# Performance work log

Measured on AMD Instinct MI355X. Metric: run time of the kernel, lower is better.

## Reference

```python
import jax, jax.numpy as jnp
import numpy as np

EPS = 1e-6
OMEGA = 0.1


def setup_inputs() -> dict:
    key = jax.random.key(0)
    k1, k2 = jax.random.split(key)
    n, d, kk = 4096, 128, 4
    inputs = jax.random.uniform(k1, (n, d), dtype=jnp.float32)  # positive so log(sim) is finite
    labels = jax.random.randint(k2, (n, kk), 0, 64, dtype=jnp.int64)
    return {"inputs": inputs, "labels": labels}


def reference(inputs, labels):
    n, kk = labels.shape
    sim = inputs @ inputs.T                      # [n, n]
    logsim = jnp.log(sim + EPS)                  # a_{jk} = log(sim[j,k]+eps)
    targets = labels[:, 0]
    eye = jnp.eye(n, dtype=bool)
    # pos_mask[j,k] = (targets[j] == targets[k]) xor diagonal
    pos = (targets[:, None] == targets[None, :]) & ~eye
    # eq[j,l,i] = (labels[l,i] == targets[j])
    eq = targets[:, None, None] == labels[None, :, :]
    m_idx = jnp.arange(kk)
    cols = kk - 1 - m_idx                        # neg_mask[m] uses label column kk-1-m
    # neg_mask[m][j,l] == 1  <=>  ~eq[j,l,kk-1-m]  AND  (m==0 or eq[j,l,kk-m])
    neq_col = ~eq[:, :, cols]                    # [j,l,m]
    prev_ok = jnp.concatenate(
        [jnp.ones((n, n, 1), dtype=bool), eq[:, :, cols[:-1]]], axis=-1)
    neg = neq_col & prev_ok                      # [j,l,m]
    # loss_pair[m] = log(Omega+eps) - log(Omega^(kk-m+1)+eps)
    lp = jnp.log(OMEGA + EPS) - jnp.log(OMEGA ** (kk - m_idx + 1) + EPS)  # [kk]
    dt = logsim.dtype
    posf = pos.astype(dt)
    negf = neg.astype(dt)
    # term = (a_jk - b_jlm)^2 with b_jlm = logsim[j,l] + 0.1*lp[m]
    # expand: sum_jklm pos*neg*(a^2 - 2ab + b^2), separable over k and (l,m)
    c = posf.sum(1)                              # [j] count of positives
    S1 = (posf * logsim).sum(1)                  # [j] sum a
    S2 = (posf * logsim ** 2).sum(1)             # [j] sum a^2
    b = logsim[:, :, None] + 0.1 * lp[None, None, :]   # [j,l,m]
    Ncnt = negf.sum(1)                           # [j,m]
    T1 = (negf * b).sum(1)                       # [j,m]
    T2 = (negf * b ** 2).sum(1)                  # [j,m]
    loss = (S2[:, None] * Ncnt - 2.0 * S1[:, None] * T1 + c[:, None] * T2).sum()
    return loss
```

## Files before the change

### kernel.cpp

```cpp
#include <hip/hip_runtime.h>
#include <math.h>

constexpr int N   = 4096;
constexpr int D   = 128;
constexpr int LDK = D + 8;
constexpr int NT  = 64;

typedef __attribute__((ext_vector_type(8))) short short8;
typedef __attribute__((ext_vector_type(4))) float floatx4;

__device__ inline unsigned short f2bf(float f) {
  unsigned u = __builtin_bit_cast(unsigned, f);
  u = (u + 0x7FFFu + ((u >> 16) & 1u)) >> 16;
  return (unsigned short)u;
}

__global__ __launch_bounds__(256) void build_coef(
    const int* __restrict__ labels, float4* __restrict__ tab,
    float B0, float B1, float B2, float B3,
    float Q0, float Q1, float Q2, float Q3) {
  const int idx = blockIdx.x * 256 + threadIdx.x;
  const int t = idx >> 12;
  const int j = idx & (N - 1);
  const int4 L = ((const int4*)labels)[j];
  const bool e0 = (t == L.x), e1 = (t == L.y), e2 = (t == L.z), e3 = (t == L.w);
  const bool n0 = !e3, n1 = e3 && !e2, n2 = e2 && !e1, n3 = e1 && !e0;
  const float g0 = (float)((n0 ? 1 : 0) + (n1 ? 1 : 0) + (n2 ? 1 : 0) + (n3 ? 1 : 0));
  const float gB = (n0 ? B0 : 0.f) + (n1 ? B1 : 0.f) + (n2 ? B2 : 0.f) + (n3 ? B3 : 0.f);
  const float gQ = (n0 ? Q0 : 0.f) + (n1 ? Q1 : 0.f) + (n2 ? Q2 : 0.f) + (n3 ? Q3 : 0.f);
  tab[idx] = make_float4(gB, gQ, g0, e0 ? 1.f : 0.f);
}

__global__ __launch_bounds__(256, 2) void logratio_phaseA(
    const float* __restrict__ inputs, const int* __restrict__ labels,
    const float4* __restrict__ tab, float* __restrict__ part) {

  __shared__ __align__(16) char smem[2 * 128 * LDK * 2];
  unsigned short* As = (unsigned short*)smem;
  unsigned short* Bs = As + 128 * LDK;
  float* Red = (float*)smem;

  const int tid = threadIdx.x;
  const int iBase = blockIdx.y * 128;
  const int jBase = blockIdx.x * 128;

#pragma unroll
  for (int p = 0; p < 16; ++p) {
    const int idx = p * 256 + tid;
    const int row = idx >> 5;
    const int cf  = idx & 31;
    const float4 va = *(const float4*)&inputs[(iBase + row) * D + cf * 4];
    uint2 wa;
    wa.x = (unsigned)f2bf(va.x) | ((unsigned)f2bf(va.y) << 16);
    wa.y = (unsigned)f2bf(va.z) | ((unsigned)f2bf(va.w) << 16);
    *(uint2*)&As[row * LDK + cf * 4] = wa;
    const float4 vb = *(const float4*)&inputs[(jBase + row) * D + cf * 4];
    uint2 wb;
    wb.x = (unsigned)f2bf(vb.x) | ((unsigned)f2bf(vb.y) << 16);
    wb.y = (unsigned)f2bf(vb.z) | ((unsigned)f2bf(vb.w) << 16);
    *(uint2*)&Bs[row * LDK + cf * 4] = wb;
  }
  __syncthreads();

  const int w    = tid >> 6;
  const int lane = tid & 63;
  const int lc   = lane & 15;
  const int quad = lane >> 4;

  floatx4 acc[2][8] = {};
  const unsigned short* Abase = As + (w * 32 + lc) * LDK + quad * 8;
  const unsigned short* Bbase = Bs + lc * LDK + quad * 8;

#pragma unroll
  for (int kb = 0; kb < 4; ++kb) {
    short8 af[2], bfr[8];
    af[0] = *(const short8*)(Abase + kb * 32);
    af[1] = *(const short8*)(Abase + 16 * LDK + kb * 32);
#pragma unroll
    for (int tn = 0; tn < 8; ++tn)
      bfr[tn] = *(const short8*)(Bbase + tn * 16 * LDK + kb * 32);
#pragma unroll
    for (int tm = 0; tm < 2; ++tm)
#pragma unroll
      for (int tn = 0; tn < 8; ++tn)
        acc[tm][tn] = __builtin_amdgcn_mfma_f32_16x16x32_bf16(af[tm], bfr[tn], acc[tm][tn], 0, 0, 0);
  }

  __syncthreads();

  const bool diag = (iBase == jBase);
#pragma unroll
  for (int tm = 0; tm < 2; ++tm) {
#pragma unroll
    for (int reg = 0; reg < 4; ++reg) {
      const int row = w * 32 + tm * 16 + quad * 4 + reg;
      const int gi = iBase + row;
      const int ti = labels[gi * 4];
      const float4* tabrow = tab + ti * N + jBase + lc;
      const int dcol = diag ? row : -1;

      float a_c = 0.f, a_s1 = 0.f, a_s2 = 0.f;
      float a_A = 0.f, a_B = 0.f, a_C = 0.f;
#pragma unroll
      for (int tn = 0; tn < 8; ++tn) {
        const float4 cf = tabrow[tn * 16];
        const float ls = __logf(acc[tm][tn][reg] + 1e-6f);
        const float t1 = fmaf(cf.z, ls, cf.x);
        a_A += cf.z;
        a_B += t1;
        a_C += fmaf(t1 + cf.x, ls, cf.y);
        const float f = (tn * 16 + lc == dcol) ? 0.f : cf.w;
        const float fls = f * ls;
        a_c += f;
        a_s1 += fls;
        a_s2 = fmaf(fls, ls, a_s2);
      }
      float* dst = Red + row * 97 + lc * 6;
      dst[0] = a_c;  dst[1] = a_s1; dst[2] = a_s2;
      dst[3] = a_A;  dst[4] = a_B;  dst[5] = a_C;
    }
  }
  __syncthreads();

  if (tid < 128) {
    const int gi = iBase + tid;
    const float* src = Red + tid * 97;
    float s0 = 0.f, s1 = 0.f, s2 = 0.f, s3 = 0.f, s4 = 0.f, s5 = 0.f;
#pragma unroll
    for (int l = 0; l < 16; ++l) {
      s0 += src[l * 6 + 0]; s1 += src[l * 6 + 1]; s2 += src[l * 6 + 2];
      s3 += src[l * 6 + 3]; s4 += src[l * 6 + 4]; s5 += src[l * 6 + 5];
    }
    float* dst = part + (size_t)gi * 256 + blockIdx.x * 8;
    *(float4*)dst       = make_float4(s0, s1, s2, s3);
    *(float2*)(dst + 4) = make_float2(s4, s5);
  }
}

__global__ __launch_bounds__(256) void logratio_phaseB(
    const float* __restrict__ part, float* __restrict__ out) {
  const int i = blockIdx.x * 256 + threadIdx.x;
  const float* p = part + (size_t)i * 256;
  float c = 0.f, S1 = 0.f, S2 = 0.f, A = 0.f, B = 0.f, C = 0.f;
#pragma unroll 8
  for (int b = 0; b < 32; ++b) {
    const float4 x = *(const float4*)(p + b * 8);
    const float2 y = *(const float2*)(p + b * 8 + 4);
    c += x.x; S1 += x.y; S2 += x.z; A += x.w; B += y.x; C += y.y;
  }
  float v = S2 * A - 2.f * S1 * B + c * C;
#pragma unroll
  for (int m = 32; m >= 1; m >>= 1) v += __shfl_xor(v, m, 64);
  __shared__ float wsum[4];
  if ((threadIdx.x & 63) == 0) wsum[threadIdx.x >> 6] = v;
  __syncthreads();
  if (threadIdx.x == 0) atomicAdd(out, wsum[0] + wsum[1] + wsum[2] + wsum[3]);
}

extern "C" void kernel_launch(void* const* d_in, const int* in_sizes, int n_in,
                              void* d_out, int out_size, void* d_ws, size_t ws_size,
                              hipStream_t stream) {
  const float* inputs = (const float*)d_in[0];
  const int* labels = (const int*)d_in[1];
  float* out = (float*)d_out;
  float4* tab = (float4*)d_ws;
  float* part = (float*)d_ws + (NT * N * 4);

  hipMemsetAsync(d_out, 0, sizeof(float), stream);

  float Bq[4], Qq[4];
  for (int m = 0; m < 4; ++m) {
    const float lpv = logf(0.1f + 1e-6f) - logf(powf(0.1f, (float)(5 - m)) + 1e-6f);
    Bq[m] = 0.1f * lpv;
    Qq[m] = Bq[m] * Bq[m];
  }

  build_coef<<<NT * N / 256, 256, 0, stream>>>(labels, tab,
                                               Bq[0], Bq[1], Bq[2], Bq[3],
                                               Qq[0], Qq[1], Qq[2], Qq[3]);
  dim3 grid(N / 128, N / 128);
  logratio_phaseA<<<grid, 256, 0, stream>>>(inputs, labels, tab, part);
  logratio_phaseB<<<N / 256, 256, 0, stream>>>(part, out);
}
```

Before: 92.46 us.

## Pre-convert inputs to swizzled bf16 and stream tiles into LDS directly

A fused prep kernel builds the coefficient table, converts the inputs to bf16 once in an XOR-swizzled layout, computes the log of each diagonal self-similarity, and zeroes the accumulators and output, replacing the memset. The main kernel uses 512 threads and loads tiles straight from global memory into LDS with global_load_lds, removing per-block fp32-to-bf16 conversion and using the swizzle to avoid bank conflicts. The diagonal exclusion moves out of the inner loop and into phase B as a subtraction. Per-row partials are combined with atomics instead of a partial buffer, which adds atomic contention and changes the floating-point summation order.

```diff
diff --git a/kernel.cpp b/kernel.cpp
--- a/kernel.cpp
+++ b/kernel.cpp
@@ -1,124 +1,143 @@
 #include <hip/hip_runtime.h>
 #include <math.h>
 
-constexpr int N   = 4096;
-constexpr int D   = 128;
-constexpr int LDK = D + 8;
-constexpr int NT  = 64;
+constexpr int N  = 4096;
+constexpr int D  = 128;
+constexpr int NT = 64;
+
+constexpr size_t TAB_OFF = 0;
+constexpr size_t XBF_OFF = (size_t)4 << 20;
+constexpr size_t ACC_OFF = (size_t)5 << 20;
+constexpr size_t LSD_OFF = ((size_t)5 << 20) + ((size_t)96 << 10);
 
 typedef __attribute__((ext_vector_type(8))) short short8;
 typedef __attribute__((ext_vector_type(4))) float floatx4;
-
-__device__ inline unsigned short f2bf(float f) {
+typedef __attribute__((address_space(1))) unsigned int gu32;
+typedef __attribute__((address_space(3))) unsigned int lu32;
+
+__device__ inline unsigned f2bf(float f) {
   unsigned u = __builtin_bit_cast(unsigned, f);
-  u = (u + 0x7FFFu + ((u >> 16) & 1u)) >> 16;
-  return (unsigned short)u;
-}
-
-__global__ __launch_bounds__(256) void build_coef(
-    const int* __restrict__ labels, float4* __restrict__ tab,
+  return (u + 0x7FFFu + ((u >> 16) & 1u)) >> 16;
+}
+
+__global__ __launch_bounds__(256) void k1_prep(
+    const float* __restrict__ X, const int* __restrict__ labels,
+    char* __restrict__ ws, float* __restrict__ out,
     float B0, float B1, float B2, float B3,
     float Q0, float Q1, float Q2, float Q3) {
-  const int idx = blockIdx.x * 256 + threadIdx.x;
-  const int t = idx >> 12;
-  const int j = idx & (N - 1);
-  const int4 L = ((const int4*)labels)[j];
-  const bool e0 = (t == L.x), e1 = (t == L.y), e2 = (t == L.z), e3 = (t == L.w);
-  const bool n0 = !e3, n1 = e3 && !e2, n2 = e2 && !e1, n3 = e1 && !e0;
-  const float g0 = (float)((n0 ? 1 : 0) + (n1 ? 1 : 0) + (n2 ? 1 : 0) + (n3 ? 1 : 0));
-  const float gB = (n0 ? B0 : 0.f) + (n1 ? B1 : 0.f) + (n2 ? B2 : 0.f) + (n3 ? B3 : 0.f);
-  const float gQ = (n0 ? Q0 : 0.f) + (n1 ? Q1 : 0.f) + (n2 ? Q2 : 0.f) + (n3 ? Q3 : 0.f);
-  tab[idx] = make_float4(gB, gQ, g0, e0 ? 1.f : 0.f);
-}
-
-__global__ __launch_bounds__(256, 2) void logratio_phaseA(
-    const float* __restrict__ inputs, const int* __restrict__ labels,
-    const float4* __restrict__ tab, float* __restrict__ part) {
-
-  __shared__ __align__(16) char smem[2 * 128 * LDK * 2];
-  unsigned short* As = (unsigned short*)smem;
-  unsigned short* Bs = As + 128 * LDK;
-  float* Red = (float*)smem;
-
-  const int tid = threadIdx.x;
-  const int iBase = blockIdx.y * 128;
-  const int jBase = blockIdx.x * 128;
-
-#pragma unroll
-  for (int p = 0; p < 16; ++p) {
-    const int idx = p * 256 + tid;
-    const int row = idx >> 5;
-    const int cf  = idx & 31;
-    const float4 va = *(const float4*)&inputs[(iBase + row) * D + cf * 4];
-    uint2 wa;
-    wa.x = (unsigned)f2bf(va.x) | ((unsigned)f2bf(va.y) << 16);
-    wa.y = (unsigned)f2bf(va.z) | ((unsigned)f2bf(va.w) << 16);
-    *(uint2*)&As[row * LDK + cf * 4] = wa;
-    const float4 vb = *(const float4*)&inputs[(jBase + row) * D + cf * 4];
-    uint2 wb;
-    wb.x = (unsigned)f2bf(vb.x) | ((unsigned)f2bf(vb.y) << 16);
-    wb.y = (unsigned)f2bf(vb.z) | ((unsigned)f2bf(vb.w) << 16);
-    *(uint2*)&Bs[row * LDK + cf * 4] = wb;
-  }
-  __syncthreads();
-
+  const int b = blockIdx.x, t = threadIdx.x;
+  if (b < 1024) {
+    const int idx = b * 256 + t;
+    const int tt = idx >> 12;
+    const int j  = idx & (N - 1);
+    const int4 L = ((const int4*)labels)[j];
+    const bool e0 = (tt == L.x), e1 = (tt == L.y), e2 = (tt == L.z), e3 = (tt == L.w);
+    const bool n0 = !e3, n1 = e3 && !e2, n2 = e2 && !e1, n3 = e1 && !e0;
+    const float g0 = (float)((n0 ? 1 : 0) + (n1 ? 1 : 0) + (n2 ? 1 : 0) + (n3 ? 1 : 0));
+    const float gB = (n0 ? B0 : 0.f) + (n1 ? B1 : 0.f) + (n2 ? B2 : 0.f) + (n3 ? B3 : 0.f);
+    const float gQ = (n0 ? Q0 : 0.f) + (n1 ? Q1 : 0.f) + (n2 ? Q2 : 0.f) + (n3 ? Q3 : 0.f);
+    ((float4*)(ws + TAB_OFF))[idx] = make_float4(gB, gQ, g0, e0 ? 1.f : 0.f);
+    if (idx < 6 * N) ((float*)(ws + ACC_OFF))[idx] = 0.f;
+  } else if (b < 1280) {
+    const int task = (b - 1024) * 256 + t;
+    const int r   = task >> 4;
+    const int blk = task & 15;
+    const float4 x0 = *(const float4*)&X[r * D + blk * 8];
+    const float4 x1 = *(const float4*)&X[r * D + blk * 8 + 4];
+    uint4 wv;
+    wv.x = f2bf(x0.x) | (f2bf(x0.y) << 16);
+    wv.y = f2bf(x0.z) | (f2bf(x0.w) << 16);
+    wv.z = f2bf(x1.x) | (f2bf(x1.y) << 16);
+    wv.w = f2bf(x1.z) | (f2bf(x1.w) << 16);
+    *(uint4*)(ws + XBF_OFF + (size_t)r * 256 + ((blk ^ (r & 15)) * 16)) = wv;
+  } else {
+    const int i = (b - 1280) * 256 + t;
+    const float* xr = X + i * D;
+    float s = 0.f;
+#pragma unroll
+    for (int c = 0; c < 32; ++c) {
+      const float4 v = ((const float4*)xr)[c];
+      s += v.x * v.x + v.y * v.y + v.z * v.z + v.w * v.w;
+    }
+    ((float*)(ws + LSD_OFF))[i] = __logf(s + 1e-6f);
+    if (b == 1295 && t == 0) out[0] = 0.f;
+  }
+}
+
+__global__ __launch_bounds__(512, 4) void logratio_phaseA(
+    const char* __restrict__ ws_ro, const int* __restrict__ labels,
+    float* acc6) {
+
+  __shared__ __align__(16) char smem[65536];
+
+  const int tid  = threadIdx.x;
   const int w    = tid >> 6;
   const int lane = tid & 63;
   const int lc   = lane & 15;
   const int quad = lane >> 4;
-
-  floatx4 acc[2][8] = {};
-  const unsigned short* Abase = As + (w * 32 + lc) * LDK + quad * 8;
-  const unsigned short* Bbase = Bs + lc * LDK + quad * 8;
-
+  const int jBase = blockIdx.x * 128;
+  const int iBase = blockIdx.y * 128;
+
+  const char* xbf = ws_ro + XBF_OFF;
+  const char* gB_ = xbf + (size_t)jBase * 256 + w * 4096 + lane * 16;
+  const char* gA_ = xbf + (size_t)iBase * 256 + w * 4096 + lane * 16;
+#pragma unroll
+  for (int c = 0; c < 4; ++c) {
+    __builtin_amdgcn_global_load_lds((const gu32*)(gB_ + c * 1024),
+                                     (lu32*)(smem + w * 4096 + c * 1024), 16, 0, 0);
+    __builtin_amdgcn_global_load_lds((const gu32*)(gA_ + c * 1024),
+                                     (lu32*)(smem + 32768 + w * 4096 + c * 1024), 16, 0, 0);
+  }
+
+  int tis[4];
+#pragma unroll
+  for (int reg = 0; reg < 4; ++reg)
+    tis[reg] = labels[(iBase + w * 16 + quad * 4 + reg) * 4];
+
+  __syncthreads();
+
+  floatx4 acc[8] = {};
+  const char* Abase = smem + 32768 + (w * 16 + lc) * 256;
 #pragma unroll
   for (int kb = 0; kb < 4; ++kb) {
-    short8 af[2], bfr[8];
-    af[0] = *(const short8*)(Abase + kb * 32);
-    af[1] = *(const short8*)(Abase + 16 * LDK + kb * 32);
+    const int pb = ((kb * 4 + quad) ^ lc) * 16;
+    const short8 af = *(const short8*)(Abase + pb);
+    short8 bfr[8];
 #pragma unroll
     for (int tn = 0; tn < 8; ++tn)
-      bfr[tn] = *(const short8*)(Bbase + tn * 16 * LDK + kb * 32);
-#pragma unroll
-    for (int tm = 0; tm < 2; ++tm)
-#pragma unroll
-      for (int tn = 0; tn < 8; ++tn)
-        acc[tm][tn] = __builtin_amdgcn_mfma_f32_16x16x32_bf16(af[tm], bfr[tn], acc[tm][tn], 0, 0, 0);
-  }
-
-  __syncthreads();
-
-  const bool diag = (iBase == jBase);
-#pragma unroll
-  for (int tm = 0; tm < 2; ++tm) {
-#pragma unroll
-    for (int reg = 0; reg < 4; ++reg) {
-      const int row = w * 32 + tm * 16 + quad * 4 + reg;
-      const int gi = iBase + row;
-      const int ti = labels[gi * 4];
-      const float4* tabrow = tab + ti * N + jBase + lc;
-      const int dcol = diag ? row : -1;
-
-      float a_c = 0.f, a_s1 = 0.f, a_s2 = 0.f;
-      float a_A = 0.f, a_B = 0.f, a_C = 0.f;
-#pragma unroll
-      for (int tn = 0; tn < 8; ++tn) {
-        const float4 cf = tabrow[tn * 16];
-        const float ls = __logf(acc[tm][tn][reg] + 1e-6f);
-        const float t1 = fmaf(cf.z, ls, cf.x);
-        a_A += cf.z;
-        a_B += t1;
-        a_C += fmaf(t1 + cf.x, ls, cf.y);
-        const float f = (tn * 16 + lc == dcol) ? 0.f : cf.w;
-        const float fls = f * ls;
-        a_c += f;
-        a_s1 += fls;
-        a_s2 = fmaf(fls, ls, a_s2);
-      }
-      float* dst = Red + row * 97 + lc * 6;
-      dst[0] = a_c;  dst[1] = a_s1; dst[2] = a_s2;
-      dst[3] = a_A;  dst[4] = a_B;  dst[5] = a_C;
+      bfr[tn] = *(const short8*)(smem + (tn * 16 + lc) * 256 + pb);
+#pragma unroll
+    for (int tn = 0; tn < 8; ++tn)
+      acc[tn] = __builtin_amdgcn_mfma_f32_16x16x32_bf16(af, bfr[tn], acc[tn], 0, 0, 0);
+  }
+
+  __syncthreads();
+  float* Red = (float*)smem;
+
+  const float4* tab = (const float4*)(ws_ro + TAB_OFF);
+#pragma unroll
+  for (int reg = 0; reg < 4; ++reg) {
+    const int row = w * 16 + quad * 4 + reg;
+    const float4* trow = tab + (size_t)tis[reg] * N + jBase + lc;
+
+    float a_c = 0.f, a_s1 = 0.f, a_s2 = 0.f;
+    float a_A = 0.f, a_B = 0.f, a_C = 0.f;
+#pragma unroll
+    for (int tn = 0; tn < 8; ++tn) {
+      const float4 cf = trow[tn * 16];
+      const float ls = __logf(acc[tn][reg] + 1e-6f);
+      const float t1 = fmaf(cf.z, ls, cf.x);
+      a_A += cf.z;
+      a_B += t1;
+      a_C += fmaf(t1 + cf.x, ls, cf.y);
+      const float fls = cf.w * ls;
+      a_c += cf.w;
+      a_s1 += fls;
+      a_s2 = fmaf(fls, ls, a_s2);
     }
+    float* dst = Red + row * 97 + lc * 6;
+    dst[0] = a_c;  dst[1] = a_s1; dst[2] = a_s2;
+    dst[3] = a_A;  dst[4] = a_B;  dst[5] = a_C;
   }
   __syncthreads();
 
@@ -131,23 +150,29 @@
       s0 += src[l * 6 + 0]; s1 += src[l * 6 + 1]; s2 += src[l * 6 + 2];
       s3 += src[l * 6 + 3]; s4 += src[l * 6 + 4]; s5 += src[l * 6 + 5];
     }
-    float* dst = part + (size_t)gi * 256 + blockIdx.x * 8;
-    *(float4*)dst       = make_float4(s0, s1, s2, s3);
-    *(float2*)(dst + 4) = make_float2(s4, s5);
+    atomicAdd(&acc6[0 * N + gi], s0);
+    atomicAdd(&acc6[1 * N + gi], s1);
+    atomicAdd(&acc6[2 * N + gi], s2);
+    atomicAdd(&acc6[3 * N + gi], s3);
+    atomicAdd(&acc6[4 * N + gi], s4);
+    atomicAdd(&acc6[5 * N + gi], s5);
   }
 }
 
 __global__ __launch_bounds__(256) void logratio_phaseB(
-    const float* __restrict__ part, float* __restrict__ out) {
+    const char* __restrict__ ws_ro, float* out) {
   const int i = blockIdx.x * 256 + threadIdx.x;
-  const float* p = part + (size_t)i * 256;
-  float c = 0.f, S1 = 0.f, S2 = 0.f, A = 0.f, B = 0.f, C = 0.f;
-#pragma unroll 8
-  for (int b = 0; b < 32; ++b) {
-    const float4 x = *(const float4*)(p + b * 8);
-    const float2 y = *(const float2*)(p + b * 8 + 4);
-    c += x.x; S1 += x.y; S2 += x.z; A += x.w; B += y.x; C += y.y;
-  }
+  const float* acc6 = (const float*)(ws_ro + ACC_OFF);
+  float c  = acc6[0 * N + i];
+  float S1 = acc6[1 * N + i];
+  float S2 = acc6[2 * N + i];
+  const float A = acc6[3 * N + i];
+  const float B = acc6[4 * N + i];
+  const float C = acc6[5 * N + i];
+  const float lsd = ((const float*)(ws_ro + LSD_OFF))[i];
+  c  -= 1.f;
+  S1 -= lsd;
+  S2 -= lsd * lsd;
   float v = S2 * A - 2.f * S1 * B + c * C;
 #pragma unroll
   for (int m = 32; m >= 1; m >>= 1) v += __shfl_xor(v, m, 64);
@@ -163,10 +188,7 @@
   const float* inputs = (const float*)d_in[0];
   const int* labels = (const int*)d_in[1];
   float* out = (float*)d_out;
-  float4* tab = (float4*)d_ws;
-  float* part = (float*)d_ws + (NT * N * 4);
-
-  hipMemsetAsync(d_out, 0, sizeof(float), stream);
+  char* ws = (char*)d_ws;
 
   float Bq[4], Qq[4];
   for (int m = 0; m < 4; ++m) {
@@ -175,10 +197,10 @@
     Qq[m] = Bq[m] * Bq[m];
   }
 
-  build_coef<<<NT * N / 256, 256, 0, stream>>>(labels, tab,
-                                               Bq[0], Bq[1], Bq[2], Bq[3],
-                                               Qq[0], Qq[1], Qq[2], Qq[3]);
+  k1_prep<<<1296, 256, 0, stream>>>(inputs, labels, ws, out,
+                                    Bq[0], Bq[1], Bq[2], Bq[3],
+                                    Qq[0], Qq[1], Qq[2], Qq[3]);
   dim3 grid(N / 128, N / 128);
-  logratio_phaseA<<<grid, 256, 0, stream>>>(inputs, labels, tab, part);
-  logratio_phaseB<<<N / 256, 256, 0, stream>>>(part, out);
-}
+  logratio_phaseA<<<grid, 512, 0, stream>>>(ws, labels, (float*)(ws + ACC_OFF));
+  logratio_phaseB<<<N / 256, 256, 0, stream>>>(ws, out);
+}
```

After: 83.91 us. 9.2% less time.
